# Performance work log

Measured on AMD Instinct MI355X. Metric: run time of the kernel, lower is better.

## Reference

```python
import jax, jax.numpy as jnp
import numpy as np
from jax import lax

B, C, H, W = 1, 512, 64, 64
HEADS, GROUPS, STRIDE, KK = 8, 4, 2, 5
HC = C // HEADS          # 64 head channels
CG = C // GROUPS         # 128 group channels
GH = HEADS // GROUPS     # 2 heads per group
OFR = 2.0                # offset_range_factor
SCALE = HC ** -0.5


def ref_points(Hk, Wk):
    # torch linspace(0.5, Hk-0.5, Hk)/Hk*2-1 == (arange+0.5)/Hk*2-1
    ry = (jnp.arange(Hk, dtype=jnp.float32) + 0.5) / Hk * 2.0 - 1.0
    rx = (jnp.arange(Wk, dtype=jnp.float32) + 0.5) / Wk * 2.0 - 1.0
    return jnp.stack(jnp.meshgrid(ry, rx, indexing='ij'), axis=-1)  # [Hk,Wk,2] (y,x)


def _gather(img, ix, iy, Hi, Wi):
    # img [N,Cc,Hi,Wi]; ix,iy float index maps [N,...]; zero padding outside
    N, Cc = img.shape[0], img.shape[1]
    valid = ((ix >= 0) & (ix <= Wi - 1) & (iy >= 0) & (iy <= Hi - 1)).astype(img.dtype)
    ixc = jnp.clip(ix, 0, Wi - 1).astype(jnp.int32)
    iyc = jnp.clip(iy, 0, Hi - 1).astype(jnp.int32)
    idx = (iyc * Wi + ixc).reshape(N, -1)
    imgf = img.reshape(N, Cc, Hi * Wi)
    g = jax.vmap(lambda im, ii: im[:, ii])(imgf, idx).reshape((N, Cc) + ix.shape[1:])
    return g * valid[:, None]


def grid_sample(img, grid):
    # bilinear, align_corners=True, zeros padding; grid [...,(x,y)] in [-1,1]
    N, Cc, Hi, Wi = img.shape
    gx = (grid[..., 0] + 1.0) * 0.5 * (Wi - 1)
    gy = (grid[..., 1] + 1.0) * 0.5 * (Hi - 1)
    x0 = jnp.floor(gx); y0 = jnp.floor(gy)
    wx = gx - x0; wy = gy - y0
    w00 = ((1 - wx) * (1 - wy))[:, None]; w01 = (wx * (1 - wy))[:, None]
    w10 = ((1 - wx) * wy)[:, None]; w11 = (wx * wy)[:, None]
    return (_gather(img, x0, y0, Hi, Wi) * w00 + _gather(img, x0 + 1, y0, Hi, Wi) * w01
            + _gather(img, x0, y0 + 1, Hi, Wi) * w10 + _gather(img, x0 + 1, y0 + 1, Hi, Wi) * w11)


def conv1x1(w, b, x):  # x [B,C,H,W]
    return jnp.einsum('oc,bchw->bohw', w, x) + b[None, :, None, None]


def setup_inputs() -> dict:
    key = jax.random.key(0)
    ks = jax.random.split(key, 8)
    d = {}
    d['x'] = jax.random.normal(ks[0], (B, C, H, W), jnp.float32)
    d['wq'] = jax.random.normal(ks[1], (C, C), jnp.float32) * 0.04
    d['bq'] = jnp.zeros((C,), jnp.float32)
    d['wk'] = jax.random.normal(ks[2], (C, C), jnp.float32) * 0.04
    d['bk'] = jnp.zeros((C,), jnp.float32)
    d['wv'] = jax.random.normal(ks[3], (C, C), jnp.float32) * 0.04
    d['bv'] = jnp.zeros((C,), jnp.float32)
    d['wo'] = jax.random.normal(ks[4], (C, C), jnp.float32) * 0.04
    d['bo'] = jnp.zeros((C,), jnp.float32)
    d['w_off_dw'] = jax.random.normal(ks[5], (CG, 1, KK, KK), jnp.float32) * 0.1
    d['b_off_dw'] = jnp.zeros((CG,), jnp.float32)
    d['ln_g'] = jnp.ones((CG,), jnp.float32)
    d['ln_b'] = jnp.zeros((CG,), jnp.float32)
    d['w_off_pw'] = jax.random.normal(ks[6], (2, CG), jnp.float32) * 0.05
    d['rpe_table'] = jax.random.normal(ks[7], (HEADS, 2 * H - 1, 2 * W - 1), jnp.float32) * 0.01
    return d


def reference(x, wq, bq, wk, bk, wv, bv, wo, bo, w_off_dw, b_off_dw, ln_g, ln_b, w_off_pw, rpe_table):
    q = conv1x1(wq, bq, x)                                   # [B,C,H,W]
    q_off = q.reshape(B * GROUPS, CG, H, W)
    # conv_offset: depthwise 5x5 stride-2 -> LayerNorm(channels) -> GELU -> 1x1 to 2ch
    t = lax.conv_general_dilated(q_off, w_off_dw, (STRIDE, STRIDE),
                                 ((KK // 2, KK // 2), (KK // 2, KK // 2)),
                                 feature_group_count=CG,
                                 dimension_numbers=('NCHW', 'OIHW', 'NCHW'))
    t = t + b_off_dw[None, :, None, None]
    mu = t.mean(1, keepdims=True)
    var = ((t - mu) ** 2).mean(1, keepdims=True)
    t = (t - mu) * lax.rsqrt(var + 1e-5) * ln_g[None, :, None, None] + ln_b[None, :, None, None]
    t = jax.nn.gelu(t, approximate=False)
    offset = jnp.einsum('oc,bchw->bohw', w_off_pw, t)        # [B*G,2,Hk,Wk]
    Hk, Wk = offset.shape[2], offset.shape[3]
    ns = Hk * Wk
    orange = jnp.array([1.0 / Hk, 1.0 / Wk], dtype=x.dtype).reshape(1, 2, 1, 1)
    offset = jnp.tanh(offset) * orange * OFR
    offset = offset.transpose(0, 2, 3, 1)                    # [B*G,Hk,Wk,2] (y,x)
    ref = jnp.broadcast_to(ref_points(Hk, Wk)[None], (B * GROUPS, Hk, Wk, 2))
    pos = offset + ref
    xs = grid_sample(x.reshape(B * GROUPS, CG, H, W), pos[..., ::-1])  # [B*G,CG,Hk,Wk]
    xs = xs.reshape(B, C, ns)
    qf = q.reshape(B * HEADS, HC, H * W)
    k = (jnp.einsum('oc,bcn->bon', wk, xs) + bk[None, :, None]).reshape(B * HEADS, HC, ns)
    v = (jnp.einsum('oc,bcn->bon', wv, xs) + bv[None, :, None]).reshape(B * HEADS, HC, ns)
    attn = jnp.einsum('bcm,bcn->bmn', qf, k) * SCALE         # [B*heads, HW, ns]
    # relative position bias via grid_sample of the rpe table
    rpe = jnp.broadcast_to(rpe_table[None], (B, HEADS, 2 * H - 1, 2 * W - 1)).reshape(
        B * GROUPS, GH, 2 * H - 1, 2 * W - 1)
    qg = jnp.broadcast_to(ref_points(H, W).reshape(1, H * W, 2), (B * GROUPS, H * W, 2))
    disp = (qg[:, :, None, :] - pos.reshape(B * GROUPS, ns, 2)[:, None, :, :]) * 0.5
    bias = grid_sample(rpe, disp[..., ::-1]).reshape(B * HEADS, H * W, ns)
    attn = jax.nn.softmax(attn + bias, axis=2)
    out = jnp.einsum('bmn,bcn->bcm', attn, v).reshape(B, C, H, W)
    y = conv1x1(wo, bo, out)
    return (y, pos.reshape(B, GROUPS, Hk, Wk, 2), ref.reshape(B, GROUPS, Hk, Wk, 2))
```

## Files before the change

kernel.cpp:

```cpp
#include <hip/hip_runtime.h>
#include <math.h>

#define CC   512
#define HH   64
#define WW   64
#define HWN  4096
#define HEADS 8
#define GROUPS 4
#define HC   64
#define CG   128
#define NS   1024
#define HK   32
#define SCALE 0.125f
#define RPE_W 127
#define RPE_N 16129

__global__ __launch_bounds__(256) void gemm_bias_kernel(
    const float* __restrict__ A, const float* __restrict__ B,
    const float* __restrict__ bias, float* __restrict__ C,
    int N, int K)
{
  __shared__ __align__(16) float As[32][64];
  __shared__ __align__(16) float Bs[32][64];
  const int bn0 = blockIdx.x * 64;
  const int bm0 = blockIdx.y * 64;
  const int tid = threadIdx.x;
  const int tx = tid & 15, ty = tid >> 4;
  float acc[4][4] = {};

  const int am = tid >> 2;
  const int ak = (tid & 3) * 8;
  const int bn = tid & 63;
  const int bk = (tid >> 6) * 8;

  for (int kt = 0; kt < K; kt += 32) {
    float4 a0 = *(const float4*)&A[(size_t)(bm0 + am) * K + kt + ak];
    float4 a1 = *(const float4*)&A[(size_t)(bm0 + am) * K + kt + ak + 4];
    As[ak + 0][am] = a0.x; As[ak + 1][am] = a0.y;
    As[ak + 2][am] = a0.z; As[ak + 3][am] = a0.w;
    As[ak + 4][am] = a1.x; As[ak + 5][am] = a1.y;
    As[ak + 6][am] = a1.z; As[ak + 7][am] = a1.w;
    #pragma unroll
    for (int r = 0; r < 8; ++r)
      Bs[bk + r][bn] = B[(size_t)(kt + bk + r) * N + bn0 + bn];
    __syncthreads();
    #pragma unroll
    for (int kk = 0; kk < 32; ++kk) {
      float4 a = *(const float4*)&As[kk][ty * 4];
      float4 b = *(const float4*)&Bs[kk][tx * 4];
      acc[0][0] += a.x * b.x; acc[0][1] += a.x * b.y; acc[0][2] += a.x * b.z; acc[0][3] += a.x * b.w;
      acc[1][0] += a.y * b.x; acc[1][1] += a.y * b.y; acc[1][2] += a.y * b.z; acc[1][3] += a.y * b.w;
      acc[2][0] += a.z * b.x; acc[2][1] += a.z * b.y; acc[2][2] += a.z * b.z; acc[2][3] += a.z * b.w;
      acc[3][0] += a.w * b.x; acc[3][1] += a.w * b.y; acc[3][2] += a.w * b.z; acc[3][3] += a.w * b.w;
    }
    __syncthreads();
  }
  #pragma unroll
  for (int i = 0; i < 4; ++i) {
    float bi = bias[bm0 + ty * 4 + i];
    #pragma unroll
    for (int j = 0; j < 4; ++j)
      C[(size_t)(bm0 + ty * 4 + i) * N + bn0 + tx * 4 + j] = acc[i][j] + bi;
  }
}

__global__ __launch_bounds__(256) void dwconv_kernel(
    const float* __restrict__ q,
    const float* __restrict__ w_dw,
    const float* __restrict__ b_dw,
    float* __restrict__ t_ws)
{
  __shared__ __align__(16) float plane[HWN];
  const int c = blockIdx.x;
  const int g = blockIdx.y;
  const int tid = threadIdx.x;

  const float* qplane = q + (size_t)(g * CG + c) * HWN;
  for (int i = tid; i < HWN / 4; i += 256)
    ((float4*)plane)[i] = ((const float4*)qplane)[i];

  float wreg[25];
  #pragma unroll
  for (int t = 0; t < 25; ++t) wreg[t] = w_dw[c * 25 + t];
  const float bias = b_dw[c];

  __syncthreads();

  #pragma unroll
  for (int k = 0; k < 4; ++k) {
    int p = (k << 8) | tid;
    int oy = p >> 5, ox = p & 31;
    int iy0 = oy * 2 - 2, ix0 = ox * 2 - 2;
    float acc = bias;
    #pragma unroll
    for (int ky = 0; ky < 5; ++ky) {
      int iy = iy0 + ky;
      bool yok = (iy >= 0) & (iy <= 63);
      int iyc = min(max(iy, 0), 63);
      #pragma unroll
      for (int kx = 0; kx < 5; ++kx) {
        int ix = ix0 + kx;
        bool ok = yok & (ix >= 0) & (ix <= 63);
        int ixc = min(max(ix, 0), 63);
        float v = plane[iyc * 64 + ixc];
        acc += wreg[ky * 5 + kx] * (ok ? v : 0.f);
      }
    }
    t_ws[(size_t)(((g << 10) | p) << 7) + c] = acc;
  }
}

__device__ __forceinline__ float block_sum_128(float v, float* red, int c) {
  red[c] = v;
  __syncthreads();
  #pragma unroll
  for (int s = 64; s > 0; s >>= 1) {
    if (c < s) red[c] += red[c + s];
    __syncthreads();
  }
  float r = red[0];
  __syncthreads();
  return r;
}

__global__ __launch_bounds__(128) void lnpw_kernel(
    const float* __restrict__ t_ws,
    const float* __restrict__ ln_g, const float* __restrict__ ln_b,
    const float* __restrict__ w_pw,
    float* __restrict__ pos_ws,
    float* __restrict__ pos_out,
    float* __restrict__ ref_out)
{
  __shared__ float red[128];
  const int blk = blockIdx.x;
  const int g = blk >> 10, p = blk & 1023;
  const int oy = p >> 5, ox = p & 31;
  const int c = threadIdx.x;

  float t = t_ws[(size_t)blk * CG + c];
  float mu = block_sum_128(t, red, c) * (1.f / 128.f);
  float d = t - mu;
  float var = block_sum_128(d * d, red, c) * (1.f / 128.f);
  float u = d * rsqrtf(var + 1e-5f) * ln_g[c] + ln_b[c];
  float ge = 0.5f * u * (1.f + erff(u * 0.70710678118654752f));
  float sy = block_sum_128(w_pw[c] * ge, red, c);
  float sx = block_sum_128(w_pw[128 + c] * ge, red, c);
  if (c == 0) {
    const float scale = 2.0f / 32.0f;
    float offy = tanhf(sy) * scale;
    float offx = tanhf(sx) * scale;
    float refy = ((float)oy + 0.5f) * (2.f / 32.f) - 1.f;
    float refx = ((float)ox + 0.5f) * (2.f / 32.f) - 1.f;
    float py = offy + refy, px = offx + refx;
    int o = (g << 10) | p;
    pos_ws[o * 2 + 0] = py;  pos_ws[o * 2 + 1] = px;
    pos_out[o * 2 + 0] = py; pos_out[o * 2 + 1] = px;
    ref_out[o * 2 + 0] = refy; ref_out[o * 2 + 1] = refx;
  }
}

__device__ __forceinline__ float tap_img(const float* __restrict__ img,
                                         float xf, float yf, float lim, int Wr) {
  bool v = (xf >= 0.f) & (xf <= lim) & (yf >= 0.f) & (yf <= lim);
  float xc = fminf(fmaxf(xf, 0.f), lim);
  float yc = fminf(fmaxf(yf, 0.f), lim);
  int ix = (int)xc, iy = (int)yc;
  float val = img[iy * Wr + ix];
  return v ? val : 0.f;
}

__global__ __launch_bounds__(256) void sample_kernel(
    const float* __restrict__ x, const float* __restrict__ pos_ws,
    float* __restrict__ xs)
{
  int t = blockIdx.x * 256 + threadIdx.x;
  int c = t >> 10;
  int p = t & 1023;
  int g = c >> 7;
  float py = pos_ws[((g << 10) | p) * 2 + 0];
  float px = pos_ws[((g << 10) | p) * 2 + 1];
  float gx = (px + 1.f) * 0.5f * 63.f;
  float gy = (py + 1.f) * 0.5f * 63.f;
  float x0 = floorf(gx), y0 = floorf(gy);
  float wx = gx - x0, wy = gy - y0;
  const float* img = x + (size_t)c * HWN;
  float v00 = tap_img(img, x0,       y0,       63.f, 64);
  float v01 = tap_img(img, x0 + 1.f, y0,       63.f, 64);
  float v10 = tap_img(img, x0,       y0 + 1.f, 63.f, 64);
  float v11 = tap_img(img, x0 + 1.f, y0 + 1.f, 63.f, 64);
  xs[(size_t)c * NS + p] =
      (v00 * (1.f - wx) + v01 * wx) * (1.f - wy) +
      (v10 * (1.f - wx) + v11 * wx) * wy;
}

__global__ __launch_bounds__(256) void attn_kernel(
    const float* __restrict__ q,
    const float* __restrict__ kb,
    const float* __restrict__ vb,
    const float* __restrict__ pos,
    const float* __restrict__ rpe,
    float* __restrict__ ob)
{
  __shared__ __align__(16) float qs[64][64];
  __shared__ __align__(16) float kv[64][68];
  __shared__ __align__(16) float ps[64][72];
  __shared__ float posn[64][2];

  const int h = blockIdx.y;
  const int m0 = blockIdx.x * 64;
  const int g = h >> 1;
  const int tid = threadIdx.x;
  const int tx = tid & 15, ty = tid >> 4;
  const float* rpeh = rpe + h * RPE_N;

  for (int i = tid; i < 64 * 64; i += 256) {
    int ch = i >> 6, m = i & 63;
    qs[ch][m] = q[(size_t)(h * HC + ch) * HWN + m0 + m];
  }

  const float qgy = ((float)(m0 >> 6) + 0.5f) * (2.f / 64.f) - 1.f;
  const float ayp = qgy * 31.5f + 63.f;
  float axp[4];
  #pragma unroll
  for (int i = 0; i < 4; ++i) {
    float qgx = ((float)(ty * 4 + i) + 0.5f) * (2.f / 64.f) - 1.f;
    axp[i] = qgx * 31.5f + 63.f;
  }

  float mrun[4], lrun[4], O[4][4];
  #pragma unroll
  for (int i = 0; i < 4; ++i) {
    mrun[i] = -INFINITY; lrun[i] = 0.f;
    #pragma unroll
    for (int j = 0; j < 4; ++j) O[i][j] = 0.f;
  }

  for (int n0 = 0; n0 < NS; n0 += 64) {
    __syncthreads();
    for (int i = tid; i < 64 * 64; i += 256) {
      int ch = i >> 6, n = i & 63;
      kv[ch][((n & 15) << 2) | (n >> 4)] = kb[(size_t)(h * HC + ch) * NS + n0 + n];
    }
    if (tid < 128)
      posn[tid >> 1][tid & 1] = pos[(size_t)((g << 10) + n0 + (tid >> 1)) * 2 + (tid & 1)];
    __syncthreads();

    float wyv[4], bxv[4];
    int   r0[4], r1[4];
    bool  yv0[4], yv1[4];
    #pragma unroll
    for (int j = 0; j < 4; ++j) {
      float py = posn[16 * j + tx][0];
      float px = posn[16 * j + tx][1];
      bxv[j] = px * 31.5f;
      float gy = ayp - py * 31.5f;
      float y0f = floorf(gy);
      wyv[j] = gy - y0f;
      yv0[j] = (y0f >= 0.f) & (y0f <= 126.f);
      yv1[j] = (y0f >= -1.f) & (y0f <= 125.f);
      int y0c = (int)fminf(fmaxf(y0f, 0.f), 126.f);
      int y1c = (int)fminf(fmaxf(y0f + 1.f, 0.f), 126.f);
      r0[j] = y0c * RPE_W;
      r1[j] = y1c * RPE_W;
    }

    float s[4][4] = {};
    #pragma unroll
    for (int ch = 0; ch < 64; ++ch) {
      float4 a = *(const float4*)&qs[ch][ty * 4];
      float4 b = *(const float4*)&kv[ch][tx * 4];
      s[0][0] += a.x * b.x; s[0][1] += a.x * b.y; s[0][2] += a.x * b.z; s[0][3] += a.x * b.w;
      s[1][0] += a.y * b.x; s[1][1] += a.y * b.y; s[1][2] += a.y * b.z; s[1][3] += a.y * b.w;
      s[2][0] += a.z * b.x; s[2][1] += a.z * b.y; s[2][2] += a.z * b.z; s[2][3] += a.z * b.w;
      s[3][0] += a.w * b.x; s[3][1] += a.w * b.y; s[3][2] += a.w * b.z; s[3][3] += a.w * b.w;
    }

    #pragma unroll
    for (int j = 0; j < 4; ++j) {
      float wy1 = wyv[j], wy0 = 1.f - wy1;
      #pragma unroll
      for (int i = 0; i < 4; ++i) {
        float gx = axp[i] - bxv[j];
        float x0f = floorf(gx);
        float wx = gx - x0f;
        bool xv0 = (x0f >= 0.f) & (x0f <= 126.f);
        bool xv1 = (x0f >= -1.f) & (x0f <= 125.f);
        int xi0 = (int)fminf(fmaxf(x0f, 0.f), 126.f);
        int xi1 = (int)fminf(fmaxf(x0f + 1.f, 0.f), 126.f);
        float t00 = rpeh[r0[j] + xi0];
        float t01 = rpeh[r0[j] + xi1];
        float t10 = rpeh[r1[j] + xi0];
        float t11 = rpeh[r1[j] + xi1];
        float v00 = (xv0 & yv0[j]) ? t00 : 0.f;
        float v01 = (xv1 & yv0[j]) ? t01 : 0.f;
        float v10 = (xv0 & yv1[j]) ? t10 : 0.f;
        float v11 = (xv1 & yv1[j]) ? t11 : 0.f;
        float bt = v00 * (1.f - wx) + v01 * wx;
        float bb = v10 * (1.f - wx) + v11 * wx;
        s[i][j] = s[i][j] * SCALE + bt * wy0 + bb * wy1;
      }
    }

    float pl[4][4];
    #pragma unroll
    for (int i = 0; i < 4; ++i) {
      float rm = fmaxf(fmaxf(s[i][0], s[i][1]), fmaxf(s[i][2], s[i][3]));
      rm = fmaxf(rm, __shfl_xor(rm, 1, 16));
      rm = fmaxf(rm, __shfl_xor(rm, 2, 16));
      rm = fmaxf(rm, __shfl_xor(rm, 4, 16));
      rm = fmaxf(rm, __shfl_xor(rm, 8, 16));
      float mnew = fmaxf(mrun[i], rm);
      float alpha = __expf(mrun[i] - mnew);
      mrun[i] = mnew;
      float rs = 0.f;
      #pragma unroll
      for (int j = 0; j < 4; ++j) {
        pl[i][j] = __expf(s[i][j] - mnew);
        rs += pl[i][j];
      }
      rs += __shfl_xor(rs, 1, 16);
      rs += __shfl_xor(rs, 2, 16);
      rs += __shfl_xor(rs, 4, 16);
      rs += __shfl_xor(rs, 8, 16);
      lrun[i] = lrun[i] * alpha + rs;
      #pragma unroll
      for (int j = 0; j < 4; ++j) O[i][j] *= alpha;
    }

    __syncthreads();
    #pragma unroll
    for (int j = 0; j < 4; ++j) {
      float4 pw;
      pw.x = pl[0][j]; pw.y = pl[1][j]; pw.z = pl[2][j]; pw.w = pl[3][j];
      *(float4*)&ps[16 * j + tx][ty * 4] = pw;
    }
    for (int i = tid; i < 64 * 64; i += 256) {
      int ch = (i & 3) | ((i >> 8) << 2);
      int n = (i >> 2) & 63;
      kv[n][ch] = vb[(size_t)(h * HC + ch) * NS + n0 + n];
    }
    __syncthreads();

    #pragma unroll
    for (int n = 0; n < 64; ++n) {
      float4 p4 = *(const float4*)&ps[n][ty * 4];
      float4 v4 = *(const float4*)&kv[n][tx * 4];
      O[0][0] += p4.x * v4.x; O[0][1] += p4.x * v4.y; O[0][2] += p4.x * v4.z; O[0][3] += p4.x * v4.w;
      O[1][0] += p4.y * v4.x; O[1][1] += p4.y * v4.y; O[1][2] += p4.y * v4.z; O[1][3] += p4.y * v4.w;
      O[2][0] += p4.z * v4.x; O[2][1] += p4.z * v4.y; O[2][2] += p4.z * v4.z; O[2][3] += p4.z * v4.w;
      O[3][0] += p4.w * v4.x; O[3][1] += p4.w * v4.y; O[3][2] += p4.w * v4.z; O[3][3] += p4.w * v4.w;
    }
  }

  __syncthreads();
  #pragma unroll
  for (int i = 0; i < 4; ++i) {
    float inv = 1.f / lrun[i];
    #pragma unroll
    for (int j = 0; j < 4; ++j)
      kv[tx * 4 + j][ty * 4 + i] = O[i][j] * inv;
  }
  __syncthreads();
  for (int i = tid; i < 64 * 64; i += 256) {
    int ch = i >> 6, m = i & 63;
    ob[(size_t)(h * HC + ch) * HWN + m0 + m] = kv[ch][m];
  }
}

extern "C" void kernel_launch(void* const* d_in, const int* in_sizes, int n_in,
                              void* d_out, int out_size, void* d_ws, size_t ws_size,
                              hipStream_t stream) {
  const float* x     = (const float*)d_in[0];
  const float* wq    = (const float*)d_in[1];
  const float* bq    = (const float*)d_in[2];
  const float* wk    = (const float*)d_in[3];
  const float* bk    = (const float*)d_in[4];
  const float* wv    = (const float*)d_in[5];
  const float* bv    = (const float*)d_in[6];
  const float* wo    = (const float*)d_in[7];
  const float* bo    = (const float*)d_in[8];
  const float* w_dw  = (const float*)d_in[9];
  const float* b_dw  = (const float*)d_in[10];
  const float* ln_g  = (const float*)d_in[11];
  const float* ln_b  = (const float*)d_in[12];
  const float* w_pw  = (const float*)d_in[13];
  const float* rpe   = (const float*)d_in[14];

  float* out = (float*)d_out;
  float* y_out   = out;
  float* pos_out = out + 2097152;
  float* ref_out = out + 2097152 + 8192;

  float* ws = (float*)d_ws;
  float* qbuf  = ws;
  float* posws = qbuf + 2097152;
  float* xsbuf = posws + 8192;
  float* kbuf  = xsbuf + 524288;
  float* vbuf  = kbuf + 524288;
  float* obuf  = vbuf + 524288;
  float* t_ws  = xsbuf;

  gemm_bias_kernel<<<dim3(HWN / 64, CC / 64), 256, 0, stream>>>(wq, x, bq, qbuf, HWN, CC);
  dwconv_kernel<<<dim3(CG, GROUPS), 256, 0, stream>>>(qbuf, w_dw, b_dw, t_ws);
  lnpw_kernel<<<dim3(GROUPS * NS), 128, 0, stream>>>(t_ws, ln_g, ln_b, w_pw,
                                                     posws, pos_out, ref_out);
  sample_kernel<<<dim3(CC * NS / 256), 256, 0, stream>>>(x, posws, xsbuf);
  gemm_bias_kernel<<<dim3(NS / 64, CC / 64), 256, 0, stream>>>(wk, xsbuf, bk, kbuf, NS, CC);
  gemm_bias_kernel<<<dim3(NS / 64, CC / 64), 256, 0, stream>>>(wv, xsbuf, bv, vbuf, NS, CC);
  attn_kernel<<<dim3(HWN / 64, HEADS), 256, 0, stream>>>(qbuf, kbuf, vbuf, posws, rpe, obuf);
  gemm_bias_kernel<<<dim3(HWN / 64, CC / 64), 256, 0, stream>>>(wo, obuf, bo, y_out, HWN, CC);
}
```

Baseline: 495.6 us.

## Run attention QK and PV on MFMA using split-fp16 hi/lo emulation

Rewrites the attention kernel so it uses MFMA 16x16x32 f16 instructions instead of scalar FP32 FMAs. Each FP32 operand is split into high and low fp16 halves, and three MFMA products are summed to keep roughly FP32 accuracy. New pre-pass kernels transpose and split K and convert V into hi/lo fp16 buffers, and these reuse workspace regions. The goal is to cut the dominant attention compute cost, at the price of extra passes and some precision risk. Q is split inside the kernel, and the probabilities are staged through swizzled shared memory to rebuild the operand layout.

```diff
diff --git a/kernel.cpp b/kernel.cpp
--- a/kernel.cpp
+++ b/kernel.cpp
@@ -1,4 +1,5 @@
 #include <hip/hip_runtime.h>
+#include <hip/hip_fp16.h>
 #include <math.h>
 
 #define CC   512
@@ -15,6 +16,9 @@
 #define RPE_W 127
 #define RPE_N 16129
 
+typedef _Float16 f16x8 __attribute__((ext_vector_type(8)));
+typedef float f32x4 __attribute__((ext_vector_type(4)));
+
 __global__ __launch_bounds__(256) void gemm_bias_kernel(
     const float* __restrict__ A, const float* __restrict__ B,
     const float* __restrict__ bias, float* __restrict__ C,
@@ -65,10 +69,8 @@
 }
 
 __global__ __launch_bounds__(256) void dwconv_kernel(
-    const float* __restrict__ q,
-    const float* __restrict__ w_dw,
-    const float* __restrict__ b_dw,
-    float* __restrict__ t_ws)
+    const float* __restrict__ q, const float* __restrict__ w_dw,
+    const float* __restrict__ b_dw, float* __restrict__ t_ws)
 {
   __shared__ __align__(16) float plane[HWN];
   const int c = blockIdx.x;
@@ -127,8 +129,7 @@
     const float* __restrict__ t_ws,
     const float* __restrict__ ln_g, const float* __restrict__ ln_b,
     const float* __restrict__ w_pw,
-    float* __restrict__ pos_ws,
-    float* __restrict__ pos_out,
+    float* __restrict__ pos_ws, float* __restrict__ pos_out,
     float* __restrict__ ref_out)
 {
   __shared__ float red[128];
@@ -193,177 +194,246 @@
       (v10 * (1.f - wx) + v11 * wx) * wy;
 }
 
+__device__ __forceinline__ void split_f16(float x, ushort& h, ushort& l) {
+  __half xh = __float2half(x);
+  float hf = __half2float(xh);
+  __half xl = __float2half(x - hf);
+  h = __half_as_ushort(xh);
+  l = __half_as_ushort(xl);
+}
+
+__global__ __launch_bounds__(256) void tsplit_kernel(
+    const float* __restrict__ src, ushort* __restrict__ dh,
+    ushort* __restrict__ dl, int ncols)
+{
+  __shared__ float tile[64][65];
+  const int ct = blockIdx.x, hh = blockIdx.y;
+  const int tid = threadIdx.x;
+  for (int i = tid; i < 4096; i += 256) {
+    int ch = i >> 6, m = i & 63;
+    tile[ch][m] = src[(size_t)(hh * 64 + ch) * ncols + ct * 64 + m];
+  }
+  __syncthreads();
+  for (int i = tid; i < 4096; i += 256) {
+    int m = i >> 6, ch = i & 63;
+    ushort h, l;
+    split_f16(tile[ch][m], h, l);
+    size_t o = ((size_t)hh * ncols + ct * 64 + m) * 64 + ch;
+    dh[o] = h; dl[o] = l;
+  }
+}
+
+__global__ __launch_bounds__(256) void vsplit_kernel(
+    const float* __restrict__ src, ushort* __restrict__ dh,
+    ushort* __restrict__ dl)
+{
+  int i = blockIdx.x * 256 + threadIdx.x;
+  ushort h, l;
+  split_f16(src[i], h, l);
+  dh[i] = h; dl[i] = l;
+}
+
 __global__ __launch_bounds__(256) void attn_kernel(
-    const float* __restrict__ q,
-    const float* __restrict__ kb,
-    const float* __restrict__ vb,
+    const float*  __restrict__ qb,
+    const ushort* __restrict__ kth, const ushort* __restrict__ ktl,
+    const ushort* __restrict__ vhb, const ushort* __restrict__ vlb,
     const float* __restrict__ pos,
     const float* __restrict__ rpe,
     float* __restrict__ ob)
 {
-  __shared__ __align__(16) float qs[64][64];
-  __shared__ __align__(16) float kv[64][68];
-  __shared__ __align__(16) float ps[64][72];
-  __shared__ float posn[64][2];
-
-  const int h = blockIdx.y;
-  const int m0 = blockIdx.x * 64;
-  const int g = h >> 1;
+  __shared__ __align__(16) uint ps32[4][16][64];
+  __shared__ float olds[4][64][17];
+
+  const int h = blockIdx.y, m0 = blockIdx.x * 64, g = h >> 1;
   const int tid = threadIdx.x;
-  const int tx = tid & 15, ty = tid >> 4;
+  const int w = tid >> 6, lane = tid & 63, l15 = lane & 15, lq = lane >> 4;
   const float* rpeh = rpe + h * RPE_N;
 
-  for (int i = tid; i < 64 * 64; i += 256) {
-    int ch = i >> 6, m = i & 63;
-    qs[ch][m] = q[(size_t)(h * HC + ch) * HWN + m0 + m];
+  const int mg = m0 + w * 16 + l15;
+  f16x8 qfh[2], qfl[2];
+  #pragma unroll
+  for (int kst = 0; kst < 2; ++kst) {
+    union { f16x8 v; ushort u[8]; } Hh, Ll;
+    #pragma unroll
+    for (int j = 0; j < 8; ++j) {
+      int ch = kst * 32 + lq * 8 + j;
+      float qv = qb[((size_t)(h * 64 + ch)) * 4096 + mg];
+      ushort hh, ll;
+      split_f16(qv, hh, ll);
+      Hh.u[j] = hh; Ll.u[j] = ll;
+    }
+    qfh[kst] = Hh.v; qfl[kst] = Ll.v;
   }
 
   const float qgy = ((float)(m0 >> 6) + 0.5f) * (2.f / 64.f) - 1.f;
   const float ayp = qgy * 31.5f + 63.f;
   float axp[4];
   #pragma unroll
-  for (int i = 0; i < 4; ++i) {
-    float qgx = ((float)(ty * 4 + i) + 0.5f) * (2.f / 64.f) - 1.f;
-    axp[i] = qgx * 31.5f + 63.f;
-  }
-
-  float mrun[4], lrun[4], O[4][4];
-  #pragma unroll
-  for (int i = 0; i < 4; ++i) {
-    mrun[i] = -INFINITY; lrun[i] = 0.f;
-    #pragma unroll
-    for (int j = 0; j < 4; ++j) O[i][j] = 0.f;
-  }
-
-  for (int n0 = 0; n0 < NS; n0 += 64) {
-    __syncthreads();
-    for (int i = tid; i < 64 * 64; i += 256) {
-      int ch = i >> 6, n = i & 63;
-      kv[ch][((n & 15) << 2) | (n >> 4)] = kb[(size_t)(h * HC + ch) * NS + n0 + n];
-    }
-    if (tid < 128)
-      posn[tid >> 1][tid & 1] = pos[(size_t)((g << 10) + n0 + (tid >> 1)) * 2 + (tid & 1)];
-    __syncthreads();
-
-    float wyv[4], bxv[4];
-    int   r0[4], r1[4];
-    bool  yv0[4], yv1[4];
-    #pragma unroll
-    for (int j = 0; j < 4; ++j) {
-      float py = posn[16 * j + tx][0];
-      float px = posn[16 * j + tx][1];
-      bxv[j] = px * 31.5f;
+  for (int r = 0; r < 4; ++r) {
+    int ml = w * 16 + lq * 4 + r;
+    float qgx = ((float)ml + 0.5f) * (2.f / 64.f) - 1.f;
+    axp[r] = qgx * 31.5f + 63.f;
+  }
+
+  float mrun[4], lrun[4];
+  f32x4 O[4];
+  #pragma unroll
+  for (int r = 0; r < 4; ++r) { mrun[r] = -INFINITY; lrun[r] = 0.f; }
+  #pragma unroll
+  for (int t = 0; t < 4; ++t) O[t] = (f32x4)0.f;
+
+  for (int c = 0; c < 16; ++c) {
+    const int n0c = c * 64;
+
+    f16x8 kfh[4][2], kfl[4][2];
+    #pragma unroll
+    for (int nt = 0; nt < 4; ++nt) {
+      const ushort* b0 = kth + ((size_t)h * 1024 + n0c + nt * 16 + l15) * 64 + lq * 8;
+      const ushort* b1 = ktl + ((size_t)h * 1024 + n0c + nt * 16 + l15) * 64 + lq * 8;
+      kfh[nt][0] = *(const f16x8*)(b0);  kfh[nt][1] = *(const f16x8*)(b0 + 32);
+      kfl[nt][0] = *(const f16x8*)(b1);  kfl[nt][1] = *(const f16x8*)(b1 + 32);
+    }
+
+    f32x4 s[4];
+    #pragma unroll
+    for (int nt = 0; nt < 4; ++nt) {
+      f32x4 acc = (f32x4)0.f;
+      acc = __builtin_amdgcn_mfma_f32_16x16x32_f16(qfh[0], kfh[nt][0], acc, 0, 0, 0);
+      acc = __builtin_amdgcn_mfma_f32_16x16x32_f16(qfh[0], kfl[nt][0], acc, 0, 0, 0);
+      acc = __builtin_amdgcn_mfma_f32_16x16x32_f16(qfl[0], kfh[nt][0], acc, 0, 0, 0);
+      acc = __builtin_amdgcn_mfma_f32_16x16x32_f16(qfh[1], kfh[nt][1], acc, 0, 0, 0);
+      acc = __builtin_amdgcn_mfma_f32_16x16x32_f16(qfh[1], kfl[nt][1], acc, 0, 0, 0);
+      acc = __builtin_amdgcn_mfma_f32_16x16x32_f16(qfl[1], kfh[nt][1], acc, 0, 0, 0);
+      s[nt] = acc;
+    }
+
+    f16x8 vfh[4][2], vfl[4][2];
+    #pragma unroll
+    for (int ct = 0; ct < 4; ++ct) {
+      const ushort* b0 = vhb + ((size_t)(h * 64 + ct * 16 + l15)) * 1024 + n0c + lq * 8;
+      const ushort* b1 = vlb + ((size_t)(h * 64 + ct * 16 + l15)) * 1024 + n0c + lq * 8;
+      vfh[ct][0] = *(const f16x8*)(b0);  vfh[ct][1] = *(const f16x8*)(b0 + 32);
+      vfl[ct][0] = *(const f16x8*)(b1);  vfl[ct][1] = *(const f16x8*)(b1 + 32);
+    }
+
+    #pragma unroll
+    for (int nt = 0; nt < 4; ++nt) {
+      int n = n0c + nt * 16 + l15;
+      float py = pos[((g << 10) | n) * 2 + 0];
+      float px = pos[((g << 10) | n) * 2 + 1];
+      float bx = px * 31.5f;
       float gy = ayp - py * 31.5f;
       float y0f = floorf(gy);
-      wyv[j] = gy - y0f;
-      yv0[j] = (y0f >= 0.f) & (y0f <= 126.f);
-      yv1[j] = (y0f >= -1.f) & (y0f <= 125.f);
-      int y0c = (int)fminf(fmaxf(y0f, 0.f), 126.f);
-      int y1c = (int)fminf(fmaxf(y0f + 1.f, 0.f), 126.f);
-      r0[j] = y0c * RPE_W;
-      r1[j] = y1c * RPE_W;
-    }
-
-    float s[4][4] = {};
-    #pragma unroll
-    for (int ch = 0; ch < 64; ++ch) {
-      float4 a = *(const float4*)&qs[ch][ty * 4];
-      float4 b = *(const float4*)&kv[ch][tx * 4];
-      s[0][0] += a.x * b.x; s[0][1] += a.x * b.y; s[0][2] += a.x * b.z; s[0][3] += a.x * b.w;
-      s[1][0] += a.y * b.x; s[1][1] += a.y * b.y; s[1][2] += a.y * b.z; s[1][3] += a.y * b.w;
-      s[2][0] += a.z * b.x; s[2][1] += a.z * b.y; s[2][2] += a.z * b.z; s[2][3] += a.z * b.w;
-      s[3][0] += a.w * b.x; s[3][1] += a.w * b.y; s[3][2] += a.w * b.z; s[3][3] += a.w * b.w;
-    }
-
-    #pragma unroll
-    for (int j = 0; j < 4; ++j) {
-      float wy1 = wyv[j], wy0 = 1.f - wy1;
-      #pragma unroll
-      for (int i = 0; i < 4; ++i) {
-        float gx = axp[i] - bxv[j];
+      float wy1 = gy - y0f, wy0 = 1.f - wy1;
+      bool yv0 = (y0f >= 0.f) & (y0f <= 126.f);
+      bool yv1 = (y0f >= -1.f) & (y0f <= 125.f);
+      int rr0 = (int)fminf(fmaxf(y0f, 0.f), 126.f) * RPE_W;
+      int rr1 = (int)fminf(fmaxf(y0f + 1.f, 0.f), 126.f) * RPE_W;
+      #pragma unroll
+      for (int r = 0; r < 4; ++r) {
+        float gx = axp[r] - bx;
         float x0f = floorf(gx);
         float wx = gx - x0f;
         bool xv0 = (x0f >= 0.f) & (x0f <= 126.f);
         bool xv1 = (x0f >= -1.f) & (x0f <= 125.f);
         int xi0 = (int)fminf(fmaxf(x0f, 0.f), 126.f);
         int xi1 = (int)fminf(fmaxf(x0f + 1.f, 0.f), 126.f);
-        float t00 = rpeh[r0[j] + xi0];
-        float t01 = rpeh[r0[j] + xi1];
-        float t10 = rpeh[r1[j] + xi0];
-        float t11 = rpeh[r1[j] + xi1];
-        float v00 = (xv0 & yv0[j]) ? t00 : 0.f;
-        float v01 = (xv1 & yv0[j]) ? t01 : 0.f;
-        float v10 = (xv0 & yv1[j]) ? t10 : 0.f;
-        float v11 = (xv1 & yv1[j]) ? t11 : 0.f;
+        float t00 = rpeh[rr0 + xi0];
+        float t01 = rpeh[rr0 + xi1];
+        float t10 = rpeh[rr1 + xi0];
+        float t11 = rpeh[rr1 + xi1];
+        float v00 = (xv0 & yv0) ? t00 : 0.f;
+        float v01 = (xv1 & yv0) ? t01 : 0.f;
+        float v10 = (xv0 & yv1) ? t10 : 0.f;
+        float v11 = (xv1 & yv1) ? t11 : 0.f;
         float bt = v00 * (1.f - wx) + v01 * wx;
         float bb = v10 * (1.f - wx) + v11 * wx;
-        s[i][j] = s[i][j] * SCALE + bt * wy0 + bb * wy1;
+        s[nt][r] = s[nt][r] * SCALE + bt * wy0 + bb * wy1;
       }
     }
 
-    float pl[4][4];
-    #pragma unroll
-    for (int i = 0; i < 4; ++i) {
-      float rm = fmaxf(fmaxf(s[i][0], s[i][1]), fmaxf(s[i][2], s[i][3]));
+    #pragma unroll
+    for (int r = 0; r < 4; ++r) {
+      float rm = fmaxf(fmaxf(s[0][r], s[1][r]), fmaxf(s[2][r], s[3][r]));
       rm = fmaxf(rm, __shfl_xor(rm, 1, 16));
       rm = fmaxf(rm, __shfl_xor(rm, 2, 16));
       rm = fmaxf(rm, __shfl_xor(rm, 4, 16));
       rm = fmaxf(rm, __shfl_xor(rm, 8, 16));
-      float mnew = fmaxf(mrun[i], rm);
-      float alpha = __expf(mrun[i] - mnew);
-      mrun[i] = mnew;
+      float mnew = fmaxf(mrun[r], rm);
+      float alpha = __expf(mrun[r] - mnew);
+      mrun[r] = mnew;
       float rs = 0.f;
       #pragma unroll
-      for (int j = 0; j < 4; ++j) {
-        pl[i][j] = __expf(s[i][j] - mnew);
-        rs += pl[i][j];
+      for (int nt = 0; nt < 4; ++nt) {
+        float p = __expf(s[nt][r] - mnew);
+        s[nt][r] = p;
+        rs += p;
       }
       rs += __shfl_xor(rs, 1, 16);
       rs += __shfl_xor(rs, 2, 16);
       rs += __shfl_xor(rs, 4, 16);
       rs += __shfl_xor(rs, 8, 16);
-      lrun[i] = lrun[i] * alpha + rs;
-      #pragma unroll
-      for (int j = 0; j < 4; ++j) O[i][j] *= alpha;
-    }
-
-    __syncthreads();
-    #pragma unroll
-    for (int j = 0; j < 4; ++j) {
-      float4 pw;
-      pw.x = pl[0][j]; pw.y = pl[1][j]; pw.z = pl[2][j]; pw.w = pl[3][j];
-      *(float4*)&ps[16 * j + tx][ty * 4] = pw;
-    }
-    for (int i = tid; i < 64 * 64; i += 256) {
-      int ch = (i & 3) | ((i >> 8) << 2);
-      int n = (i >> 2) & 63;
-      kv[n][ch] = vb[(size_t)(h * HC + ch) * NS + n0 + n];
-    }
-    __syncthreads();
-
-    #pragma unroll
-    for (int n = 0; n < 64; ++n) {
-      float4 p4 = *(const float4*)&ps[n][ty * 4];
-      float4 v4 = *(const float4*)&kv[n][tx * 4];
-      O[0][0] += p4.x * v4.x; O[0][1] += p4.x * v4.y; O[0][2] += p4.x * v4.z; O[0][3] += p4.x * v4.w;
-      O[1][0] += p4.y * v4.x; O[1][1] += p4.y * v4.y; O[1][2] += p4.y * v4.z; O[1][3] += p4.y * v4.w;
-      O[2][0] += p4.z * v4.x; O[2][1] += p4.z * v4.y; O[2][2] += p4.z * v4.z; O[2][3] += p4.z * v4.w;
-      O[3][0] += p4.w * v4.x; O[3][1] += p4.w * v4.y; O[3][2] += p4.w * v4.z; O[3][3] += p4.w * v4.w;
-    }
-  }
-
-  __syncthreads();
-  #pragma unroll
-  for (int i = 0; i < 4; ++i) {
-    float inv = 1.f / lrun[i];
-    #pragma unroll
-    for (int j = 0; j < 4; ++j)
-      kv[tx * 4 + j][ty * 4 + i] = O[i][j] * inv;
-  }
-  __syncthreads();
-  for (int i = tid; i < 64 * 64; i += 256) {
-    int ch = i >> 6, m = i & 63;
-    ob[(size_t)(h * HC + ch) * HWN + m0 + m] = kv[ch][m];
+      lrun[r] = lrun[r] * alpha + rs;
+      #pragma unroll
+      for (int ct = 0; ct < 4; ++ct) O[ct][r] *= alpha;
+    }
+
+    #pragma unroll
+    for (int nt = 0; nt < 4; ++nt) {
+      #pragma unroll
+      for (int r = 0; r < 4; ++r) {
+        ushort hh, ll;
+        split_f16(s[nt][r], hh, ll);
+        uint packed = (uint)hh | ((uint)ll << 16);
+        int m = lq * 4 + r;
+        int n = nt * 16 + l15;
+        ps32[w][m][(n & 3) | ((((n >> 2) ^ m) & 15) << 2)] = packed;
+      }
+    }
+
+    f16x8 pfh[2], pfl[2];
+    #pragma unroll
+    for (int nst = 0; nst < 2; ++nst) {
+      int s0 = nst * 8 + lq * 2;
+      uint4 u0 = *(const uint4*)&ps32[w][l15][((s0 ^ l15) & 15) << 2];
+      uint4 u1 = *(const uint4*)&ps32[w][l15][(((s0 + 1) ^ l15) & 15) << 2];
+      union { f16x8 v; ushort u[8]; } ah, al;
+      uint t0[8] = {u0.x, u0.y, u0.z, u0.w, u1.x, u1.y, u1.z, u1.w};
+      #pragma unroll
+      for (int j = 0; j < 8; ++j) {
+        ah.u[j] = (ushort)(t0[j] & 0xffffu);
+        al.u[j] = (ushort)(t0[j] >> 16);
+      }
+      pfh[nst] = ah.v;
+      pfl[nst] = al.v;
+    }
+
+    #pragma unroll
+    for (int ct = 0; ct < 4; ++ct) {
+      f32x4 acc = O[ct];
+      acc = __builtin_amdgcn_mfma_f32_16x16x32_f16(pfh[0], vfh[ct][0], acc, 0, 0, 0);
+      acc = __builtin_amdgcn_mfma_f32_16x16x32_f16(pfh[0], vfl[ct][0], acc, 0, 0, 0);
+      acc = __builtin_amdgcn_mfma_f32_16x16x32_f16(pfl[0], vfh[ct][0], acc, 0, 0, 0);
+      acc = __builtin_amdgcn_mfma_f32_16x16x32_f16(pfh[1], vfh[ct][1], acc, 0, 0, 0);
+      acc = __builtin_amdgcn_mfma_f32_16x16x32_f16(pfh[1], vfl[ct][1], acc, 0, 0, 0);
+      acc = __builtin_amdgcn_mfma_f32_16x16x32_f16(pfl[1], vfh[ct][1], acc, 0, 0, 0);
+      O[ct] = acc;
+    }
+  }
+
+  float inv[4];
+  #pragma unroll
+  for (int r = 0; r < 4; ++r) inv[r] = 1.f / lrun[r];
+  #pragma unroll
+  for (int ct = 0; ct < 4; ++ct)
+    #pragma unroll
+    for (int r = 0; r < 4; ++r)
+      olds[w][ct * 16 + l15][lq * 4 + r] = O[ct][r] * inv[r];
+
+  #pragma unroll
+  for (int it = 0; it < 16; ++it) {
+    int ch = it * 4 + lq;
+    ob[((size_t)(h * 64 + ch)) * 4096 + m0 + w * 16 + l15] = olds[w][ch][l15];
   }
 }
 
@@ -399,6 +469,10 @@
   float* vbuf  = kbuf + 524288;
   float* obuf  = vbuf + 524288;
   float* t_ws  = xsbuf;
+  ushort* kth = (ushort*)xsbuf;
+  ushort* ktl = kth + 524288;
+  ushort* vhb = (ushort*)kbuf;
+  ushort* vlb = vhb + 524288;
 
   gemm_bias_kernel<<<dim3(HWN / 64, CC / 64), 256, 0, stream>>>(wq, x, bq, qbuf, HWN, CC);
   dwconv_kernel<<<dim3(CG, GROUPS), 256, 0, stream>>>(qbuf, w_dw, b_dw, t_ws);
@@ -407,6 +481,9 @@
   sample_kernel<<<dim3(CC * NS / 256), 256, 0, stream>>>(x, posws, xsbuf);
   gemm_bias_kernel<<<dim3(NS / 64, CC / 64), 256, 0, stream>>>(wk, xsbuf, bk, kbuf, NS, CC);
   gemm_bias_kernel<<<dim3(NS / 64, CC / 64), 256, 0, stream>>>(wv, xsbuf, bv, vbuf, NS, CC);
-  attn_kernel<<<dim3(HWN / 64, HEADS), 256, 0, stream>>>(qbuf, kbuf, vbuf, posws, rpe, obuf);
+  tsplit_kernel<<<dim3(NS / 64, HEADS), 256, 0, stream>>>(kbuf, kth, ktl, NS);
+  vsplit_kernel<<<dim3(CC * NS / 256), 256, 0, stream>>>(vbuf, vhb, vlb);
+  attn_kernel<<<dim3(HWN / 64, HEADS), 256, 0, stream>>>(qbuf, kth, ktl,
+                                                         vhb, vlb, posws, rpe, obuf);
   gemm_bias_kernel<<<dim3(HWN / 64, CC / 64), 256, 0, stream>>>(wo, obuf, bo, y_out, HWN, CC);
 }
```

After: 415.1 us. 1.19x faster.
